# Optimization experiments

Measured on AMD Instinct MI355X. Metric: run time of the kernel, lower is better.

The kernel has to match this reference:

```python
import jax, jax.numpy as jnp
import numpy as np

NUM_HEADS = 16


def setup_inputs() -> dict:
    key = jax.random.key(0)
    ks = jax.random.split(key, 8)
    B_, N, C = 2048, 64, 512
    nW = 64
    return {
        "x": jax.random.normal(ks[0], (B_, N, C), dtype=jnp.float32),
        "pe": jax.random.normal(ks[1], (1, N, C), dtype=jnp.float32),
        "rpe": jax.random.normal(ks[2], (NUM_HEADS, N, N), dtype=jnp.float32),
        "mask": jax.random.normal(ks[3], (nW, N, N), dtype=jnp.float32),
        "qkv_w": jax.random.normal(ks[4], (3 * C, C), dtype=jnp.float32) * 0.02,
        "qkv_b": jax.random.normal(ks[5], (3 * C,), dtype=jnp.float32) * 0.02,
        "proj_w": jax.random.normal(ks[6], (C, C), dtype=jnp.float32) * 0.02,
        "proj_b": jax.random.normal(ks[7], (C,), dtype=jnp.float32) * 0.02,
    }


def reference(x, pe, rpe, mask, qkv_w, qkv_b, proj_w, proj_b):
    B_, N, C = x.shape
    H = NUM_HEADS
    hd = C // H
    scale = hd ** -0.5
    xp = x + pe  # (B_, N, C)
    qkv = xp @ qkv_w.T + qkv_b  # (B_, N, 3C)
    qkv = qkv.reshape(B_, N, 3, H, hd).transpose(2, 0, 3, 1, 4)  # (3, B_, H, N, hd)
    q, k, v = qkv[0], qkv[1], qkv[2]
    attn = jnp.einsum("bhnd,bhmd->bhnm", q * scale, k)  # (B_, H, N, N)
    attn = attn + rpe[None]  # broadcast rpe over batch
    nW = mask.shape[0]
    attn = attn.reshape(B_ // nW, nW, H, N, N) + mask[None, :, None]
    attn = attn.reshape(B_, H, N, N)
    attn = jax.nn.softmax(attn, axis=-1)
    out = jnp.einsum("bhnm,bhmd->bhnd", attn, v)  # (B_, H, N, hd)
    out = out.transpose(0, 2, 1, 3).reshape(B_, N, C)
    return out @ proj_w.T + proj_b
```

## Files before the change

kernel.cpp:

```cpp
#include <hip/hip_runtime.h>
#include <hip/hip_bf16.h>
#include <cstdint>

typedef __bf16 bf16;
typedef __bf16 bf16x8_t __attribute__((ext_vector_type(8)));
typedef __bf16 bf16x4_t __attribute__((ext_vector_type(4)));
typedef float  f32x4_t  __attribute__((ext_vector_type(4)));

#define MFMA16(a, b, c) __builtin_amdgcn_mfma_f32_16x16x32_bf16((a), (b), (c), 0, 0, 0)

__device__ __forceinline__ void gload_lds16(const bf16* g, bf16* l) {
    __builtin_amdgcn_global_load_lds(
        (const __attribute__((address_space(1))) void*)g,
        (__attribute__((address_space(3))) void*)l,
        16, 0, 0);
}

__global__ void k_wprep(const float* __restrict__ wq, const float* __restrict__ wp,
                        bf16* __restrict__ wqb, bf16* __restrict__ wpb) {
    int t = blockIdx.x * 256 + threadIdx.x;
    int stride = gridDim.x * 256;
    for (int i = t; i < 196608; i += stride) {
        float4 v = ((const float4*)wq)[i];
        bf16x4_t o; o[0]=(bf16)v.x; o[1]=(bf16)v.y; o[2]=(bf16)v.z; o[3]=(bf16)v.w;
        ((bf16x4_t*)wqb)[i] = o;
    }
    for (int i = t; i < 65536; i += stride) {
        float4 v = ((const float4*)wp)[i];
        bf16x4_t o; o[0]=(bf16)v.x; o[1]=(bf16)v.y; o[2]=(bf16)v.z; o[3]=(bf16)v.w;
        ((bf16x4_t*)wpb)[i] = o;
    }
}

__global__ void k_xprep(const float* __restrict__ x, const float* __restrict__ pe,
                        bf16* __restrict__ xp) {
    int t = blockIdx.x * 256 + threadIdx.x;
    int stride = gridDim.x * 256;
    for (int i = t; i < 8388608; i += stride) {
        int row = i >> 6;
        int g   = (i & 63) * 8;
        const float* xr = x  + ((size_t)row << 9) + g;
        const float* pr = pe + ((size_t)(row & 63) << 9) + g;
        float4 x0 = *(const float4*)(xr);
        float4 x1 = *(const float4*)(xr + 4);
        float4 p0 = *(const float4*)(pr);
        float4 p1 = *(const float4*)(pr + 4);
        bf16x8_t v;
        v[0]=(bf16)(x0.x+p0.x); v[1]=(bf16)(x0.y+p0.y);
        v[2]=(bf16)(x0.z+p0.z); v[3]=(bf16)(x0.w+p0.w);
        v[4]=(bf16)(x1.x+p1.x); v[5]=(bf16)(x1.y+p1.y);
        v[6]=(bf16)(x1.z+p1.z); v[7]=(bf16)(x1.w+p1.w);
        *(bf16x8_t*)(xp + (size_t)i * 8) = v;
    }
}

__global__ __launch_bounds__(512, 2) void k_qkv(
    const bf16*  __restrict__ A,
    const bf16*  __restrict__ Bw,
    const float* __restrict__ bias,
    bf16* __restrict__ Cq)
{
    __shared__ bf16 As[2][256 * 64];
    __shared__ bf16 Bs[2][256 * 64];

    const int tid  = threadIdx.x;
    const int lane = tid & 63;
    const int wave = tid >> 6;
    const int lr = lane & 15, lg = lane >> 4;
    const int wr = wave >> 2;
    const int wc = wave & 3;
    const int bid = blockIdx.x;
    const int wg  = (bid & 7) * 96 + (bid >> 3);
    const int mb  = wg / 6, nb = wg - mb * 6;
    const size_t m0 = (size_t)mb * 256;
    const int n0 = nb * 256;

    f32x4_t acc[8][4] = {};

    auto stage = [&](int kt, int buf) {
        const int k0 = kt * 64;
#pragma unroll
        for (int ii = 0; ii < 4; ++ii) {
            int instr = wave * 4 + ii;
            int r  = instr * 8 + (lane >> 3);
            int gp = (lane & 7) ^ (r & 7);
            gload_lds16(A  + (m0 + r) * 512 + k0 + gp * 8, &As[buf][instr * 512]);
            gload_lds16(Bw + (size_t)(n0 + r) * 512 + k0 + gp * 8, &Bs[buf][instr * 512]);
        }
    };

    stage(0, 0);

    for (int kt = 0; kt < 8; ++kt) {
        const int cur = kt & 1;
        if (kt < 7) {
            stage(kt + 1, cur ^ 1);
            asm volatile("s_waitcnt vmcnt(8) lgkmcnt(0)" ::: "memory");
        } else {
            asm volatile("s_waitcnt vmcnt(0) lgkmcnt(0)" ::: "memory");
        }
        __builtin_amdgcn_sched_barrier(0);
        __builtin_amdgcn_s_barrier();
        __builtin_amdgcn_sched_barrier(0);

#pragma unroll
        for (int k2 = 0; k2 < 2; ++k2) {
            bf16x8_t af[8], bfr[4];
#pragma unroll
            for (int i = 0; i < 8; ++i) {
                int rowa = wr * 128 + i * 16 + lr;
                int ph   = (k2 * 4 + lg) ^ (rowa & 7);
                af[i] = *(const bf16x8_t*)&As[cur][rowa * 64 + ph * 8];
            }
#pragma unroll
            for (int j = 0; j < 4; ++j) {
                int rowb = n0 ? 0 : 0, dummy = 0; (void)dummy;
                int rb   = wc * 64 + j * 16 + lr;
                int ph   = (k2 * 4 + lg) ^ (rb & 7);
                bfr[j] = *(const bf16x8_t*)&Bs[cur][rb * 64 + ph * 8];
            }
#pragma unroll
            for (int i = 0; i < 8; ++i)
#pragma unroll
                for (int j = 0; j < 4; ++j)
                    acc[i][j] = MFMA16(af[i], bfr[j], acc[i][j]);
        }

        if (kt < 7) {
            asm volatile("s_waitcnt lgkmcnt(0)" ::: "memory");
            __builtin_amdgcn_sched_barrier(0);
            __builtin_amdgcn_s_barrier();
            __builtin_amdgcn_sched_barrier(0);
        }
    }

    float bj[4];
#pragma unroll
    for (int j = 0; j < 4; ++j) bj[j] = bias[n0 + wc * 64 + j * 16 + lr];
#pragma unroll
    for (int i = 0; i < 8; ++i)
#pragma unroll
        for (int j = 0; j < 4; ++j) {
            int col   = n0 + wc * 64 + j * 16 + lr;
            int which = col >> 9;
            int h     = (col >> 5) & 15;
            int d     = col & 31;
            bf16* base = Cq + (size_t)(which * 16 + h) * (512 * 2048);
#pragma unroll
            for (int r = 0; r < 4; ++r) {
                int mrow = (int)m0 + wr * 128 + i * 16 + lg * 4 + r;
                int win = mrow >> 6, tok = mrow & 63;
                base[(size_t)win * 2048 + tok * 32 + d] = (bf16)(acc[i][j][r] + bj[j]);
            }
        }
}

__global__ __launch_bounds__(256, 2) void k_attn(
    const bf16*  __restrict__ qkv,
    const float* __restrict__ rpe,
    const float* __restrict__ mask,
    bf16* __restrict__ ao,
    int winbase)
{
    __shared__ bf16 vts[4][32 * 72];
    __shared__ bf16 ps[4][64 * 72];

    const int tid  = threadIdx.x;
    const int lane = tid & 63;
    const int wave = tid >> 6;
    const int lr   = lane & 15;
    const int lg   = lane >> 4;
    const int bw   = blockIdx.x;
    const int gw   = winbase + bw;
    const int wi   = gw & 63;
    const float* mp = mask + (size_t)wi * 4096;
    bf16* pvt = &vts[wave][0];
    bf16* pps = &ps[wave][0];

    const float SCALE = 0.17677669529663687f;

    for (int hh = 0; hh < 4; ++hh) {
        const int h  = wave * 4 + hh;
        const float* rp = rpe + (size_t)h * 4096;
        const bf16* qb = qkv + ((size_t)(h)      * 512 + bw) * 2048;
        const bf16* kb = qkv + ((size_t)(16 + h) * 512 + bw) * 2048;
        const bf16* vb = qkv + ((size_t)(32 + h) * 512 + bw) * 2048;

        bf16x8_t qf[4], kf[4];
#pragma unroll
        for (int t = 0; t < 4; ++t) {
            qf[t] = *(const bf16x8_t*)(qb + (t * 16 + lr) * 32 + lg * 8);
            kf[t] = *(const bf16x8_t*)(kb + (t * 16 + lr) * 32 + lg * 8);
        }
#pragma unroll
        for (int j = 0; j < 4; ++j) {
            bf16x8_t vr = *(const bf16x8_t*)(vb + (j * 16 + (lane >> 2)) * 32 + (lane & 3) * 8);
#pragma unroll
            for (int i = 0; i < 8; ++i)
                pvt[((lane & 3) * 8 + i) * 72 + j * 16 + (lane >> 2)] = vr[i];
        }

        float sminv[4][4];
#pragma unroll
        for (int mt = 0; mt < 4; ++mt) {
            f32x4_t s[4];
            f32x4_t zero = {};
#pragma unroll
            for (int nt = 0; nt < 4; ++nt)
                s[nt] = MFMA16(qf[mt], kf[nt], zero);
            float rm[4][4];
#pragma unroll
            for (int nt = 0; nt < 4; ++nt) {
                int col = nt * 16 + lr;
#pragma unroll
                for (int r = 0; r < 4; ++r) {
                    int rrow = mt * 16 + lg * 4 + r;
                    rm[nt][r] = rp[rrow * 64 + col] + mp[rrow * 64 + col];
                }
            }
            float mx[4] = {-1e30f, -1e30f, -1e30f, -1e30f};
#pragma unroll
            for (int nt = 0; nt < 4; ++nt)
#pragma unroll
                for (int r = 0; r < 4; ++r) {
                    float tv = s[nt][r] * SCALE + rm[nt][r];
                    s[nt][r] = tv;
                    mx[r] = fmaxf(mx[r], tv);
                }
#pragma unroll
            for (int r = 0; r < 4; ++r) {
                float m = mx[r];
                m = fmaxf(m, __shfl_xor(m, 1));
                m = fmaxf(m, __shfl_xor(m, 2));
                m = fmaxf(m, __shfl_xor(m, 4));
                m = fmaxf(m, __shfl_xor(m, 8));
                mx[r] = m;
            }
            float sm[4] = {0.f, 0.f, 0.f, 0.f};
#pragma unroll
            for (int nt = 0; nt < 4; ++nt)
#pragma unroll
                for (int r = 0; r < 4; ++r) {
                    float e = __expf(s[nt][r] - mx[r]);
                    s[nt][r] = e;
                    sm[r] += e;
                }
#pragma unroll
            for (int r = 0; r < 4; ++r) {
                float ssum = sm[r];
                ssum += __shfl_xor(ssum, 1);
                ssum += __shfl_xor(ssum, 2);
                ssum += __shfl_xor(ssum, 4);
                ssum += __shfl_xor(ssum, 8);
                sminv[mt][r] = 1.0f / ssum;
            }
#pragma unroll
            for (int nt = 0; nt < 4; ++nt)
#pragma unroll
                for (int r = 0; r < 4; ++r)
                    pps[(mt * 16 + lg * 4 + r) * 72 + nt * 16 + lr] = (bf16)s[nt][r];
        }

#pragma unroll
        for (int mt = 0; mt < 4; ++mt) {
            f32x4_t o[2] = {};
#pragma unroll
            for (int ks = 0; ks < 2; ++ks) {
                bf16x8_t pa = *(const bf16x8_t*)&pps[(mt * 16 + lr) * 72 + ks * 32 + lg * 8];
#pragma unroll
                for (int jd = 0; jd < 2; ++jd) {
                    bf16x8_t bv = *(const bf16x8_t*)&pvt[(jd * 16 + lr) * 72 + ks * 32 + lg * 8];
                    o[jd] = MFMA16(pa, bv, o[jd]);
                }
            }
#pragma unroll
            for (int jd = 0; jd < 2; ++jd)
#pragma unroll
                for (int r = 0; r < 4; ++r) {
                    size_t rrow = (size_t)gw * 64 + mt * 16 + lg * 4 + r;
                    ao[rrow * 512 + h * 32 + jd * 16 + lr] = (bf16)(o[jd][r] * sminv[mt][r]);
                }
        }
    }
}

__global__ __launch_bounds__(512, 2) void k_proj(
    const bf16* __restrict__ A, const bf16* __restrict__ Bw,
    const float* __restrict__ bias, float* __restrict__ C)
{
    __shared__ bf16 As[2][256 * 64];
    __shared__ bf16 Bs[2][256 * 64];

    const int tid  = threadIdx.x;
    const int lane = tid & 63;
    const int wave = tid >> 6;
    const int lr = lane & 15, lg = lane >> 4;
    const int wr = wave >> 2, wc = wave & 3;
    const int bid = blockIdx.x;
    const int wg  = (bid & 7) * 128 + (bid >> 3);
    const int mb = wg >> 1, nb = wg & 1;
    const size_t m0 = (size_t)mb * 256;
    const int n0 = nb * 256;

    f32x4_t acc[8][4] = {};

    auto stage = [&](int kt, int buf) {
        const int k0 = kt * 64;
#pragma unroll
        for (int ii = 0; ii < 4; ++ii) {
            int instr = wave * 4 + ii;
            int r  = instr * 8 + (lane >> 3);
            int gp = (lane & 7) ^ (r & 7);
            gload_lds16(A  + (m0 + r) * 512 + k0 + gp * 8, &As[buf][instr * 512]);
            gload_lds16(Bw + (size_t)(n0 + r) * 512 + k0 + gp * 8, &Bs[buf][instr * 512]);
        }
    };

    stage(0, 0);

    for (int kt = 0; kt < 8; ++kt) {
        const int cur = kt & 1;
        if (kt < 7) {
            stage(kt + 1, cur ^ 1);
            asm volatile("s_waitcnt vmcnt(8) lgkmcnt(0)" ::: "memory");
        } else {
            asm volatile("s_waitcnt vmcnt(0) lgkmcnt(0)" ::: "memory");
        }
        __builtin_amdgcn_sched_barrier(0);
        __builtin_amdgcn_s_barrier();
        __builtin_amdgcn_sched_barrier(0);

#pragma unroll
        for (int k2 = 0; k2 < 2; ++k2) {
            bf16x8_t af[8], bfr[4];
#pragma unroll
            for (int i = 0; i < 8; ++i) {
                int rowa = wr * 128 + i * 16 + lr;
                int ph   = (k2 * 4 + lg) ^ (rowa & 7);
                af[i] = *(const bf16x8_t*)&As[cur][rowa * 64 + ph * 8];
            }
#pragma unroll
            for (int j = 0; j < 4; ++j) {
                int rb = wc * 64 + j * 16 + lr;
                int ph = (k2 * 4 + lg) ^ (rb & 7);
                bfr[j] = *(const bf16x8_t*)&Bs[cur][rb * 64 + ph * 8];
            }
#pragma unroll
            for (int i = 0; i < 8; ++i)
#pragma unroll
                for (int j = 0; j < 4; ++j)
                    acc[i][j] = MFMA16(af[i], bfr[j], acc[i][j]);
        }

        if (kt < 7) {
            asm volatile("s_waitcnt lgkmcnt(0)" ::: "memory");
            __builtin_amdgcn_sched_barrier(0);
            __builtin_amdgcn_s_barrier();
            __builtin_amdgcn_sched_barrier(0);
        }
    }

    float bj[4];
#pragma unroll
    for (int j = 0; j < 4; ++j) bj[j] = bias[n0 + wc * 64 + j * 16 + lr];
#pragma unroll
    for (int i = 0; i < 8; ++i)
#pragma unroll
        for (int j = 0; j < 4; ++j) {
            int col = n0 + wc * 64 + j * 16 + lr;
#pragma unroll
            for (int r = 0; r < 4; ++r) {
                size_t rw = m0 + wr * 128 + i * 16 + lg * 4 + r;
                C[rw * 512 + col] = acc[i][j][r] + bj[j];
            }
        }
}

extern "C" void kernel_launch(void* const* d_in, const int* in_sizes, int n_in,
                              void* d_out, int out_size, void* d_ws, size_t ws_size,
                              hipStream_t stream) {
    (void)in_sizes; (void)n_in; (void)out_size; (void)ws_size;
    const float* x      = (const float*)d_in[0];
    const float* pe     = (const float*)d_in[1];
    const float* rpe    = (const float*)d_in[2];
    const float* mask   = (const float*)d_in[3];
    const float* qkv_w  = (const float*)d_in[4];
    const float* qkv_b  = (const float*)d_in[5];
    const float* proj_w = (const float*)d_in[6];
    const float* proj_b = (const float*)d_in[7];
    float* out = (float*)d_out;

    char* ws = (char*)d_ws;
    bf16* wqkvb  = (bf16*)ws;
    bf16* wprojb = (bf16*)(ws + 1572864);
    bf16* ao     = (bf16*)(ws + 2097152);

    bf16* xp   = (bf16*)d_out;
    bf16* qkvc = (bf16*)((char*)d_out + 134217728);

    k_wprep<<<256, 256, 0, stream>>>(qkv_w, proj_w, wqkvb, wprojb);
    k_xprep<<<4096, 256, 0, stream>>>(x, pe, xp);
    for (int c = 0; c < 4; ++c) {
        k_qkv<<<768, 512, 0, stream>>>(xp + (size_t)c * 32768 * 512,
                                       wqkvb, qkv_b, qkvc);
        k_attn<<<512, 256, 0, stream>>>(qkvc, rpe, mask, ao, c * 512);
    }
    k_proj<<<1024, 512, 0, stream>>>(ao, wprojb, proj_b, out);
}
```

Before: 712.4 us.

## Deepen GEMM LDS pipeline to four stages with K=32 tiles

The QKV and projection GEMMs move from a double-buffered K=64 tile to a four-buffer ring of K=32 tiles with three loads in flight, each tracked by graded vmcnt waits. The LDS swizzle is redone for 4 chunks per row, and s_setprio raises wave priority around the MFMA block. The attention kernel's LDS row padding drops from 72 to 68 to change bank mapping. More iterations and barriers per tile are paid to hide global-load latency better.

```diff
diff --git a/kernel.cpp b/kernel.cpp
--- a/kernel.cpp
+++ b/kernel.cpp
@@ -60,8 +60,8 @@
     const float* __restrict__ bias,
     bf16* __restrict__ Cq)
 {
-    __shared__ bf16 As[2][256 * 64];
-    __shared__ bf16 Bs[2][256 * 64];
+    __shared__ bf16 As[4][256 * 32];
+    __shared__ bf16 Bs[4][256 * 32];
 
     const int tid  = threadIdx.x;
     const int lane = tid & 63;
@@ -75,63 +75,62 @@
     const size_t m0 = (size_t)mb * 256;
     const int n0 = nb * 256;
 
+    const int srow = lane >> 2;
+    const int sgp  = (lane & 3) ^ (srow & 3);
+
     f32x4_t acc[8][4] = {};
 
     auto stage = [&](int kt, int buf) {
-        const int k0 = kt * 64;
-#pragma unroll
-        for (int ii = 0; ii < 4; ++ii) {
-            int instr = wave * 4 + ii;
-            int r  = instr * 8 + (lane >> 3);
-            int gp = (lane & 7) ^ (r & 7);
-            gload_lds16(A  + (m0 + r) * 512 + k0 + gp * 8, &As[buf][instr * 512]);
-            gload_lds16(Bw + (size_t)(n0 + r) * 512 + k0 + gp * 8, &Bs[buf][instr * 512]);
+        const int k0 = kt * 32;
+#pragma unroll
+        for (int ii = 0; ii < 2; ++ii) {
+            int instr = wave * 2 + ii;
+            int row = instr * 16 + srow;
+            gload_lds16(A  + (m0 + row) * 512 + k0 + sgp * 8, &As[buf][instr * 512]);
+            gload_lds16(Bw + (size_t)(n0 + row) * 512 + k0 + sgp * 8, &Bs[buf][instr * 512]);
         }
     };
 
-    stage(0, 0);
-
-    for (int kt = 0; kt < 8; ++kt) {
-        const int cur = kt & 1;
-        if (kt < 7) {
-            stage(kt + 1, cur ^ 1);
-            asm volatile("s_waitcnt vmcnt(8) lgkmcnt(0)" ::: "memory");
+    stage(0, 0); stage(1, 1); stage(2, 2);
+
+    const int phr = (lg ^ (lr & 3)) * 8;
+
+    for (int kt = 0; kt < 16; ++kt) {
+        const int cur = kt & 3;
+        if (kt < 13) {
+            stage(kt + 3, (kt + 3) & 3);
+            asm volatile("s_waitcnt vmcnt(12)" ::: "memory");
+        } else if (kt == 13) {
+            asm volatile("s_waitcnt vmcnt(8)" ::: "memory");
+        } else if (kt == 14) {
+            asm volatile("s_waitcnt vmcnt(4)" ::: "memory");
         } else {
-            asm volatile("s_waitcnt vmcnt(0) lgkmcnt(0)" ::: "memory");
+            asm volatile("s_waitcnt vmcnt(0)" ::: "memory");
         }
         __builtin_amdgcn_sched_barrier(0);
         __builtin_amdgcn_s_barrier();
         __builtin_amdgcn_sched_barrier(0);
 
-#pragma unroll
-        for (int k2 = 0; k2 < 2; ++k2) {
-            bf16x8_t af[8], bfr[4];
-#pragma unroll
-            for (int i = 0; i < 8; ++i) {
-                int rowa = wr * 128 + i * 16 + lr;
-                int ph   = (k2 * 4 + lg) ^ (rowa & 7);
-                af[i] = *(const bf16x8_t*)&As[cur][rowa * 64 + ph * 8];
-            }
-#pragma unroll
-            for (int j = 0; j < 4; ++j) {
-                int rowb = n0 ? 0 : 0, dummy = 0; (void)dummy;
-                int rb   = wc * 64 + j * 16 + lr;
-                int ph   = (k2 * 4 + lg) ^ (rb & 7);
-                bfr[j] = *(const bf16x8_t*)&Bs[cur][rb * 64 + ph * 8];
-            }
-#pragma unroll
-            for (int i = 0; i < 8; ++i)
-#pragma unroll
-                for (int j = 0; j < 4; ++j)
-                    acc[i][j] = MFMA16(af[i], bfr[j], acc[i][j]);
-        }
-
-        if (kt < 7) {
-            asm volatile("s_waitcnt lgkmcnt(0)" ::: "memory");
-            __builtin_amdgcn_sched_barrier(0);
-            __builtin_amdgcn_s_barrier();
-            __builtin_amdgcn_sched_barrier(0);
-        }
+        bf16x8_t af[8], bfr[4];
+#pragma unroll
+        for (int i = 0; i < 8; ++i)
+            af[i] = *(const bf16x8_t*)&As[cur][(wr * 128 + i * 16 + lr) * 32 + phr];
+#pragma unroll
+        for (int j = 0; j < 4; ++j)
+            bfr[j] = *(const bf16x8_t*)&Bs[cur][(wc * 64 + j * 16 + lr) * 32 + phr];
+
+        __builtin_amdgcn_s_setprio(1);
+#pragma unroll
+        for (int i = 0; i < 8; ++i)
+#pragma unroll
+            for (int j = 0; j < 4; ++j)
+                acc[i][j] = MFMA16(af[i], bfr[j], acc[i][j]);
+        __builtin_amdgcn_s_setprio(0);
+
+        asm volatile("s_waitcnt lgkmcnt(0)" ::: "memory");
+        __builtin_amdgcn_sched_barrier(0);
+        __builtin_amdgcn_s_barrier();
+        __builtin_amdgcn_sched_barrier(0);
     }
 
     float bj[4];
@@ -155,6 +154,7 @@
         }
 }
 
+#define APAD 68
 __global__ __launch_bounds__(256, 2) void k_attn(
     const bf16*  __restrict__ qkv,
     const float* __restrict__ rpe,
@@ -162,8 +162,8 @@
     bf16* __restrict__ ao,
     int winbase)
 {
-    __shared__ bf16 vts[4][32 * 72];
-    __shared__ bf16 ps[4][64 * 72];
+    __shared__ bf16 vts[4][32 * APAD];
+    __shared__ bf16 ps[4][64 * APAD];
 
     const int tid  = threadIdx.x;
     const int lane = tid & 63;
@@ -197,7 +197,7 @@
             bf16x8_t vr = *(const bf16x8_t*)(vb + (j * 16 + (lane >> 2)) * 32 + (lane & 3) * 8);
 #pragma unroll
             for (int i = 0; i < 8; ++i)
-                pvt[((lane & 3) * 8 + i) * 72 + j * 16 + (lane >> 2)] = vr[i];
+                pvt[((lane & 3) * 8 + i) * APAD + j * 16 + (lane >> 2)] = vr[i];
         }
 
         float sminv[4][4];
@@ -258,7 +258,7 @@
             for (int nt = 0; nt < 4; ++nt)
 #pragma unroll
                 for (int r = 0; r < 4; ++r)
-                    pps[(mt * 16 + lg * 4 + r) * 72 + nt * 16 + lr] = (bf16)s[nt][r];
+                    pps[(mt * 16 + lg * 4 + r) * APAD + nt * 16 + lr] = (bf16)s[nt][r];
         }
 
 #pragma unroll
@@ -266,10 +266,10 @@
             f32x4_t o[2] = {};
 #pragma unroll
             for (int ks = 0; ks < 2; ++ks) {
-                bf16x8_t pa = *(const bf16x8_t*)&pps[(mt * 16 + lr) * 72 + ks * 32 + lg * 8];
+                bf16x8_t pa = *(const bf16x8_t*)&pps[(mt * 16 + lr) * APAD + ks * 32 + lg * 8];
 #pragma unroll
                 for (int jd = 0; jd < 2; ++jd) {
-                    bf16x8_t bv = *(const bf16x8_t*)&pvt[(jd * 16 + lr) * 72 + ks * 32 + lg * 8];
+                    bf16x8_t bv = *(const bf16x8_t*)&pvt[(jd * 16 + lr) * APAD + ks * 32 + lg * 8];
                     o[jd] = MFMA16(pa, bv, o[jd]);
                 }
             }
@@ -288,8 +288,8 @@
     const bf16* __restrict__ A, const bf16* __restrict__ Bw,
     const float* __restrict__ bias, float* __restrict__ C)
 {
-    __shared__ bf16 As[2][256 * 64];
-    __shared__ bf16 Bs[2][256 * 64];
+    __shared__ bf16 As[4][256 * 32];
+    __shared__ bf16 Bs[4][256 * 32];
 
     const int tid  = threadIdx.x;
     const int lane = tid & 63;
@@ -302,62 +302,62 @@
     const size_t m0 = (size_t)mb * 256;
     const int n0 = nb * 256;
 
+    const int srow = lane >> 2;
+    const int sgp  = (lane & 3) ^ (srow & 3);
+
     f32x4_t acc[8][4] = {};
 
     auto stage = [&](int kt, int buf) {
-        const int k0 = kt * 64;
-#pragma unroll
-        for (int ii = 0; ii < 4; ++ii) {
-            int instr = wave * 4 + ii;
-            int r  = instr * 8 + (lane >> 3);
-            int gp = (lane & 7) ^ (r & 7);
-            gload_lds16(A  + (m0 + r) * 512 + k0 + gp * 8, &As[buf][instr * 512]);
-            gload_lds16(Bw + (size_t)(n0 + r) * 512 + k0 + gp * 8, &Bs[buf][instr * 512]);
+        const int k0 = kt * 32;
+#pragma unroll
+        for (int ii = 0; ii < 2; ++ii) {
+            int instr = wave * 2 + ii;
+            int row = instr * 16 + srow;
+            gload_lds16(A  + (m0 + row) * 512 + k0 + sgp * 8, &As[buf][instr * 512]);
+            gload_lds16(Bw + (size_t)(n0 + row) * 512 + k0 + sgp * 8, &Bs[buf][instr * 512]);
         }
     };
 
-    stage(0, 0);
-
-    for (int kt = 0; kt < 8; ++kt) {
-        const int cur = kt & 1;
-        if (kt < 7) {
-            stage(kt + 1, cur ^ 1);
-            asm volatile("s_waitcnt vmcnt(8) lgkmcnt(0)" ::: "memory");
+    stage(0, 0); stage(1, 1); stage(2, 2);
+
+    const int phr = (lg ^ (lr & 3)) * 8;
+
+    for (int kt = 0; kt < 16; ++kt) {
+        const int cur = kt & 3;
+        if (kt < 13) {
+            stage(kt + 3, (kt + 3) & 3);
+            asm volatile("s_waitcnt vmcnt(12)" ::: "memory");
+        } else if (kt == 13) {
+            asm volatile("s_waitcnt vmcnt(8)" ::: "memory");
+        } else if (kt == 14) {
+            asm volatile("s_waitcnt vmcnt(4)" ::: "memory");
         } else {
-            asm volatile("s_waitcnt vmcnt(0) lgkmcnt(0)" ::: "memory");
+            asm volatile("s_waitcnt vmcnt(0)" ::: "memory");
         }
         __builtin_amdgcn_sched_barrier(0);
         __builtin_amdgcn_s_barrier();
         __builtin_amdgcn_sched_barrier(0);
 
-#pragma unroll
-        for (int k2 = 0; k2 < 2; ++k2) {
-            bf16x8_t af[8], bfr[4];
-#pragma unroll
-            for (int i = 0; i < 8; ++i) {
-                int rowa = wr * 128 + i * 16 + lr;
-                int ph   = (k2 * 4 + lg) ^ (rowa & 7);
-                af[i] = *(const bf16x8_t*)&As[cur][rowa * 64 + ph * 8];
-            }
-#pragma unroll
-            for (int j = 0; j < 4; ++j) {
-                int rb = wc * 64 + j * 16 + lr;
-                int ph = (k2 * 4 + lg) ^ (rb & 7);
-                bfr[j] = *(const bf16x8_t*)&Bs[cur][rb * 64 + ph * 8];
-            }
-#pragma unroll
-            for (int i = 0; i < 8; ++i)
-#pragma unroll
-                for (int j = 0; j < 4; ++j)
-                    acc[i][j] = MFMA16(af[i], bfr[j], acc[i][j]);
-        }
-
-        if (kt < 7) {
-            asm volatile("s_waitcnt lgkmcnt(0)" ::: "memory");
-            __builtin_amdgcn_sched_barrier(0);
-            __builtin_amdgcn_s_barrier();
-            __builtin_amdgcn_sched_barrier(0);
-        }
+        bf16x8_t af[8], bfr[4];
+#pragma unroll
+        for (int i = 0; i < 8; ++i)
+            af[i] = *(const bf16x8_t*)&As[cur][(wr * 128 + i * 16 + lr) * 32 + phr];
+#pragma unroll
+        for (int j = 0; j < 4; ++j)
+            bfr[j] = *(const bf16x8_t*)&Bs[cur][(wc * 64 + j * 16 + lr) * 32 + phr];
+
+        __builtin_amdgcn_s_setprio(1);
+#pragma unroll
+        for (int i = 0; i < 8; ++i)
+#pragma unroll
+            for (int j = 0; j < 4; ++j)
+                acc[i][j] = MFMA16(af[i], bfr[j], acc[i][j]);
+        __builtin_amdgcn_s_setprio(0);
+
+        asm volatile("s_waitcnt lgkmcnt(0)" ::: "memory");
+        __builtin_amdgcn_sched_barrier(0);
+        __builtin_amdgcn_s_barrier();
+        __builtin_amdgcn_sched_barrier(0);
     }
 
     float bj[4];
```

Result: slower. 827.1 us (+16.1%).
